# Kernel optimization log

Hardware: AMD Instinct MI355X
Metric: run time of the kernel (lower is better)

The kernel has to match this reference:

```python
import jax, jax.numpy as jnp
import numpy as np

B, T, D = 2, 4096, 2048
H, DK, DV, LR = 16, 128, 128, 16
GATE_NORM = 16.0
EPS = 1e-5
SCALE = DK ** -0.5

_PROJS = [("q", D, H * DK), ("k", D, H * DK), ("v", D, H * DV), ("g", D, H * DV), ("o", H * DV, D), ("gk0", D, LR), ("gk1", LR, H * DK)]


def setup_inputs() -> dict:
    key = jax.random.key(0)
    inp = {}
    k0, key = jax.random.split(key)
    inp["hidden_states"] = jax.random.normal(k0, (B, T, D), jnp.float32)
    for name, ind, outd in _PROJS:
        kw, ks, key = jax.random.split(key, 3)
        # int4 weights in [-8, 7], per-output-channel fp scale
        inp[name + "_w"] = jax.random.randint(kw, (outd, ind), -8, 8, dtype=jnp.int32)
        inp[name + "_wscale"] = jax.random.uniform(ks, (outd,), jnp.float32, 0.005, 0.02)
        inp[name + "_ascale"] = jnp.float32(0.05)  # per-tensor int8 activation scale
    kb, key = jax.random.split(key)
    inp["gk1_bias"] = jax.random.normal(kb, (H * DK,), jnp.float32) * 0.5
    inp["g_norm_weight"] = jnp.ones((DV,), jnp.float32)
    return inp


def _qlinear(x, w_int, wscale, ascale):
    # W4A8B16O16: symmetric per-tensor int8 activation quant (straight-through),
    # int4 weights dequantized with per-out-channel scale, fp accumulate/output.
    xq = jnp.clip(jnp.round(x / ascale), -128, 127) * ascale
    x_ste = x + jax.lax.stop_gradient(xq - x)
    w = w_int.astype(jnp.float32) * wscale[:, None]  # [out, in]
    return x_ste @ w.T


def _gla_scan(q, k, v, gk):
    # chunk_gla semantics: S_t = diag(exp(gk_t)) S_{t-1} + k_t v_t^T; o_t = (q_t * DK^-0.5) S_t
    # q,k,gk: [B,T,H,DK]; v: [B,T,H,DV]
    tm = lambda a: jnp.swapaxes(a, 0, 1)  # time-major [T,B,H,d]

    def step(S, x):
        qt, kt, vt, gt = x
        S = jnp.exp(gt)[..., None] * S + kt[..., None] * vt[..., None, :]
        return S, jnp.einsum('bhk,bhkv->bhv', qt, S)

    S0 = jnp.zeros((B, H, DK, DV), q.dtype)
    _, o = jax.lax.scan(step, S0, (tm(q) * SCALE, tm(k), tm(v), tm(gk)))
    return jnp.swapaxes(o, 0, 1)  # [B,T,H,DV]


def reference(hidden_states, q_w, q_wscale, q_ascale, k_w, k_wscale, k_ascale, v_w, v_wscale, v_ascale, g_w, g_wscale, g_ascale, o_w, o_wscale, o_ascale, gk0_w, gk0_wscale, gk0_ascale, gk1_w, gk1_wscale, gk1_ascale, gk1_bias, g_norm_weight):
    x = hidden_states
    q = _qlinear(x, q_w, q_wscale, q_ascale)
    k = _qlinear(x, k_w, k_wscale, k_ascale)
    v = _qlinear(x, v_w, v_wscale, v_ascale)
    gk = _qlinear(_qlinear(x, gk0_w, gk0_wscale, gk0_ascale), gk1_w, gk1_wscale, gk1_ascale) + gk1_bias
    rs = lambda a, d: a.reshape(*a.shape[:-1], -1, d)  # '... (h d) -> ... h d'
    q, k, gk, v = rs(q, DK), rs(k, DK), rs(gk, DK), rs(v, DV)
    gk = jax.nn.log_sigmoid(gk) / GATE_NORM
    o = _gla_scan(q, k, v, gk)
    g = rs(_qlinear(x, g_w, g_wscale, g_ascale), DV)
    # FusedRMSNormSwishGate: per-head rmsnorm(o) * weight, gated by swish(g)
    o = o * jax.lax.rsqrt(jnp.mean(o * o, axis=-1, keepdims=True) + EPS) * g_norm_weight
    o = o * (g * jax.nn.sigmoid(g))
    o = o.reshape(B, T, H * DV)
    return _qlinear(o, o_w, o_wscale, o_ascale)
```

## Files before the change

kernel.cpp:

```cpp
#include <hip/hip_runtime.h>

typedef __attribute__((ext_vector_type(4))) float f32x4;
typedef __attribute__((ext_vector_type(8))) short short8;
typedef __attribute__((ext_vector_type(4))) short short4v;
typedef __attribute__((ext_vector_type(4))) int int4v;
typedef __attribute__((ext_vector_type(8))) char char8;
typedef __attribute__((ext_vector_type(16))) char char16;
typedef unsigned int uint32;

#define DEVFN static __device__ __forceinline__
#define MFMA16x16x32 __builtin_amdgcn_mfma_f32_16x16x32_bf16
#define MFMA_I8 __builtin_amdgcn_mfma_i32_16x16x64_i8

DEVFN short f2bf_rn(float f) {
  uint32 u = __float_as_uint(f);
  u += 0x7FFFu + ((u >> 16) & 1u);
  return (short)(u >> 16);
}
DEVFN float bf2f(short s) { return __uint_as_float(((uint32)(unsigned short)s) << 16); }
DEVFN float quant1(float v, float as) {
  return fminf(fmaxf(rintf(v / as), -128.f), 127.f);
}
DEVFN void store1(float* p, float v) { *p = v; }
DEVFN void store1(short* p, float v) { *p = f2bf_rn(v); }

DEVFN void gload_lds16(const void* g, void* l) {
  __builtin_amdgcn_global_load_lds((const __attribute__((address_space(1))) void*)g,
                                   (__attribute__((address_space(3))) void*)l, 16, 0, 0);
}

__global__ __launch_bounds__(256) void repack_w_kernel(const int* __restrict__ w,
                                                       char* __restrict__ wq, int n16) {
  int stride = gridDim.x * blockDim.x;
  for (int i = blockIdx.x * blockDim.x + threadIdx.x; i < n16; i += stride) {
    char16 o;
#pragma unroll
    for (int s = 0; s < 4; s++) {
      int4v v = ((const int4v*)w)[i * 4 + s];
#pragma unroll
      for (int j = 0; j < 4; j++) o[s * 4 + j] = (char)v[j];
    }
    ((char16*)wq)[i] = o;
  }
}

__global__ __launch_bounds__(256) void quant5_kernel(
    const float* __restrict__ x, char* __restrict__ o_q, char* __restrict__ o_k,
    char* __restrict__ o_v, char* __restrict__ o_g, char* __restrict__ o_gk,
    const float* __restrict__ as_q, const float* __restrict__ as_k,
    const float* __restrict__ as_v, const float* __restrict__ as_g,
    const float* __restrict__ as_gk, int n8) {
  float aq = as_q[0], ak = as_k[0], av = as_v[0], ag = as_g[0], agk = as_gk[0];
  int stride = gridDim.x * blockDim.x;
  for (int i = blockIdx.x * blockDim.x + threadIdx.x; i < n8; i += stride) {
    f32x4 a = ((const f32x4*)x)[i * 2];
    f32x4 b = ((const f32x4*)x)[i * 2 + 1];
    float v[8] = {a.x, a.y, a.z, a.w, b.x, b.y, b.z, b.w};
    char8 q8, k8, v8, g8, gk8;
#pragma unroll
    for (int j = 0; j < 8; j++) {
      q8[j] = (char)(int)quant1(v[j], aq);
      k8[j] = (char)(int)quant1(v[j], ak);
      v8[j] = (char)(int)quant1(v[j], av);
      g8[j] = (char)(int)quant1(v[j], ag);
      gk8[j] = (char)(int)quant1(v[j], agk);
    }
    ((char8*)o_q)[i] = q8;
    ((char8*)o_k)[i] = k8;
    ((char8*)o_v)[i] = v8;
    ((char8*)o_g)[i] = g8;
    ((char8*)o_gk)[i] = gk8;
  }
}

template <typename OutT>
__global__ __launch_bounds__(512, 2) void gemm_i8(const char* __restrict__ A,
                                                  const char* __restrict__ W,
                                                  OutT* __restrict__ C,
                                                  const float* __restrict__ wscale,
                                                  const float* __restrict__ ascale_p) {
  const int K = 2048, N = 2048, NT = 32;
  int wg = blockIdx.x;
  int swz = (wg & 7) * 32 + (wg >> 3);
  int bm = swz >> 3, bn = swz & 7;

  __shared__ char As[2][256 * 64] __attribute__((aligned(16)));
  __shared__ char Bs[2][256 * 64] __attribute__((aligned(16)));

  int tid = threadIdx.x, lane = tid & 63, wid = tid >> 6;
  int wr = wid >> 2, wc = wid & 3;
  int ll = lane & 15, lh = lane >> 4;

  int4v acc[8][4];
#pragma unroll
  for (int m = 0; m < 8; m++)
#pragma unroll
    for (int n = 0; n < 4; n++) acc[m][n] = (int4v){0, 0, 0, 0};

  const char* Abase = A + (size_t)(bm * 256) * K;
  const char* Wbase = W + (size_t)(bn * 256) * K;

#define STAGE(buf, kt)                                                                   \
  {                                                                                      \
    _Pragma("unroll") for (int i = 0; i < 2; i++) {                                      \
      int rr = i * 128 + (tid >> 2);                                                     \
      int scc = (tid & 3) ^ ((rr >> 1) & 3);                                             \
      int ub = (i * 512 + wid * 64) * 16;                                                \
      gload_lds16(Abase + (size_t)rr * K + (kt) * 64 + scc * 16, (char*)As[buf] + ub);   \
      gload_lds16(Wbase + (size_t)rr * K + (kt) * 64 + scc * 16, (char*)Bs[buf] + ub);   \
    }                                                                                    \
  }

  STAGE(0, 0);
  STAGE(1, 1);
  int cur = 0;
  for (int kt = 0; kt < NT; kt++) {
    if (kt < NT - 1)
      asm volatile("s_waitcnt vmcnt(4)" ::: "memory");
    else
      asm volatile("s_waitcnt vmcnt(0)" ::: "memory");
    __builtin_amdgcn_s_barrier();
    asm volatile("" ::: "memory");
    int4v af[8], bfv[4];
#pragma unroll
    for (int m = 0; m < 8; m++) {
      int row = wr * 128 + m * 16 + ll;
      af[m] = *(const int4v*)(As[cur] + row * 64 + ((lh ^ ((row >> 1) & 3)) * 16));
    }
#pragma unroll
    for (int n = 0; n < 4; n++) {
      int row = wc * 64 + n * 16 + ll;
      bfv[n] = *(const int4v*)(Bs[cur] + row * 64 + ((lh ^ ((row >> 1) & 3)) * 16));
    }
    __builtin_amdgcn_s_setprio(1);
#pragma unroll
    for (int m = 0; m < 8; m++)
#pragma unroll
      for (int n = 0; n < 4; n++) acc[m][n] = MFMA_I8(af[m], bfv[n], acc[m][n], 0, 0, 0);
    __builtin_amdgcn_s_setprio(0);
    asm volatile("" ::: "memory");
    __builtin_amdgcn_s_barrier();
    if (kt + 2 < NT) STAGE(cur, kt + 2);
    cur ^= 1;
  }
  float as = ascale_p[0];
#pragma unroll
  for (int n = 0; n < 4; n++) {
    int col = bn * 256 + wc * 64 + n * 16 + ll;
    float sc = as * wscale[col];
#pragma unroll
    for (int m = 0; m < 8; m++) {
      int r0 = bm * 256 + wr * 128 + m * 16 + lh * 4;
#pragma unroll
      for (int j = 0; j < 4; j++) store1(C + (size_t)(r0 + j) * N + col, (float)acc[m][n][j] * sc);
    }
  }
#undef STAGE
}

__global__ __launch_bounds__(256) void gk0_kernel(const char* __restrict__ xq,
                                                  const int* __restrict__ w0,
                                                  const float* __restrict__ w0s,
                                                  const float* __restrict__ as_p,
                                                  float* __restrict__ inner) {
  const int K = 2048;
  __shared__ char W8[16 * 2064] __attribute__((aligned(16)));
  __shared__ char As[2][64 * 64] __attribute__((aligned(16)));

  int tid = threadIdx.x, lane = tid & 63, wid = tid >> 6;
  int ll = lane & 15, lh = lane >> 4;
  int bm = blockIdx.x;

#pragma unroll
  for (int i = 0; i < 32; i++) {
    int idx = i * 256 + tid;
    int4v v = ((const int4v*)w0)[idx];
    int e = idx * 4;
    char* p = W8 + (e >> 11) * 2064 + (e & 2047);
    p[0] = (char)v.x;
    p[1] = (char)v.y;
    p[2] = (char)v.z;
    p[3] = (char)v.w;
  }

  const char* Abase = xq + (size_t)(bm * 64) * K;
#define STAGEA(buf, kt)                                                              \
  {                                                                                  \
    int rr = tid >> 2, cc = tid & 3;                                                 \
    int ub = wid * 64 * 16;                                                          \
    gload_lds16(Abase + (size_t)rr * K + (kt) * 64 + cc * 16, (char*)As[buf] + ub);  \
  }

  int4v acc = (int4v){0, 0, 0, 0};
  STAGEA(0, 0);
  __syncthreads();
  int cur = 0;
  for (int kt = 0; kt < 32; kt++) {
    if (kt + 1 < 32) STAGEA(cur ^ 1, kt + 1);
    int4v bfv = *(const int4v*)(W8 + ll * 2064 + kt * 64 + lh * 16);
    int4v af = *(const int4v*)(As[cur] + (wid * 16 + ll) * 64 + lh * 16);
    acc = MFMA_I8(af, bfv, acc, 0, 0, 0);
    __syncthreads();
    cur ^= 1;
  }
  float sc = as_p[0] * w0s[ll];
  int r0 = bm * 64 + wid * 16 + lh * 4;
#pragma unroll
  for (int j = 0; j < 4; j++) inner[(size_t)(r0 + j) * 16 + ll] = (float)acc[j] * sc;
#undef STAGEA
}

__global__ __launch_bounds__(256) void gk1_kernel(const float* __restrict__ inner,
                                                  const int* __restrict__ w1,
                                                  const float* __restrict__ w1s,
                                                  const float* __restrict__ as_p,
                                                  const float* __restrict__ bias,
                                                  float* __restrict__ glog) {
  __shared__ float xq1[8][16] __attribute__((aligned(16)));
  float as = as_p[0];
  int tid = threadIdx.x;
  int m0 = blockIdx.x * 8;
  if (tid < 128) {
    int t = tid >> 4, n = tid & 15;
    xq1[t][n] = quant1(inner[(size_t)(m0 + t) * 16 + n], as);
  }
  __syncthreads();
#pragma unroll
  for (int i = 0; i < 8; i++) {
    int j = tid + i * 256;
    const int* wr = w1 + (size_t)j * 16;
    f32x4 wv[4];
#pragma unroll
    for (int n4 = 0; n4 < 4; n4++) {
      int4v wi = *(const int4v*)(wr + n4 * 4);
      wv[n4] = (f32x4){(float)wi.x, (float)wi.y, (float)wi.z, (float)wi.w};
    }
    float sc = as * w1s[j];
    float bj = bias[j];
#pragma unroll
    for (int t = 0; t < 8; t++) {
      f32x4 a4 = {0.f, 0.f, 0.f, 0.f};
#pragma unroll
      for (int n4 = 0; n4 < 4; n4++) a4 += *(const f32x4*)&xq1[t][n4 * 4] * wv[n4];
      float raw = (a4.x + a4.y + a4.z + a4.w) * sc + bj;
      float y = __expf(-fabsf(raw));
      float ls = fminf(raw, 0.f) - __logf(1.f + y);
      glog[(size_t)(m0 + t) * 2048 + j] = ls * 0.0625f;
    }
  }
}

__global__ __launch_bounds__(256) void phaseA_kernel(const float* __restrict__ Abuf,
                                                     const short* __restrict__ Kb,
                                                     const short* __restrict__ Vb,
                                                     short* __restrict__ U,
                                                     float* __restrict__ CT) {
  __shared__ short k2[16 * 128] __attribute__((aligned(16)));
  __shared__ short v2[16 * 128] __attribute__((aligned(16)));
  __shared__ short kt2[128 * 24] __attribute__((aligned(16)));
  __shared__ short vt2[128 * 24] __attribute__((aligned(16)));
  __shared__ float a_lds[16 * 136] __attribute__((aligned(16)));
  __shared__ float etot[128];

  int cid = blockIdx.x;
  int bb = cid >> 9, h = (cid >> 5) & 15, c = cid & 31;
  size_t rowbase = ((size_t)bb * 4096 + (size_t)c * 128) * 2048 + h * 128;
  int tid = threadIdx.x, lane = tid & 63, wid = tid >> 6;
  int lh = lane >> 4, ll = lane & 15;
  int r = tid >> 4, d0 = (tid & 15) * 8;

  f32x4 acc[8][2];
#pragma unroll
  for (int tm = 0; tm < 8; tm++) {
    acc[tm][0] = (f32x4){0.f, 0.f, 0.f, 0.f};
    acc[tm][1] = (f32x4){0.f, 0.f, 0.f, 0.f};
  }
  float ct[8] = {0.f, 0.f, 0.f, 0.f, 0.f, 0.f, 0.f, 0.f};

  for (int sb = 0; sb < 8; sb++) {
    __syncthreads();
    size_t ridx = rowbase + (size_t)(sb * 16 + r) * 2048 + d0;
    short8 k8 = *(const short8*)(Kb + ridx);
    short8 v8 = *(const short8*)(Vb + ridx);
    {
      f32x4 a0 = *(const f32x4*)(Abuf + ridx);
      f32x4 a1 = *(const f32x4*)(Abuf + ridx + 4);
      *(f32x4*)(a_lds + r * 136 + d0) = a0;
      *(f32x4*)(a_lds + r * 136 + d0 + 4) = a1;
    }
    __syncthreads();
    if (tid < 128) {
      int d = tid;
      float s = 0.f;
#pragma unroll
      for (int rr = 0; rr < 16; rr++) {
        s += a_lds[rr * 136 + d];
        a_lds[rr * 136 + d] = s;
      }
    }
    __syncthreads();
    {
      short8 ko;
#pragma unroll
      for (int j = 0; j < 8; j++) {
        float arel = a_lds[r * 136 + d0 + j];
        ko[j] = f2bf_rn(bf2f(k8[j]) * __expf(-arel));
        if (r == 15) {
          etot[d0 + j] = __expf(arel);
          ct[j] += arel;
        }
      }
      int byt = (r * 256 + d0 * 2) ^ ((r & 7) << 4);
      *(short8*)((char*)k2 + byt) = ko;
      *(short8*)((char*)v2 + byt) = v8;
    }
    __syncthreads();
    {
      int trow = tid >> 1, sh = (tid & 1) * 8;
      short8 tk, tv;
#pragma unroll
      for (int ss = 0; ss < 8; ss++) {
        int s = sh + ss;
        int eidx = ((s * 256 + trow * 2) ^ ((s & 7) << 4)) >> 1;
        tk[ss] = k2[eidx];
        tv[ss] = v2[eidx];
      }
      *(short8*)(kt2 + trow * 24 + sh) = tk;
      *(short8*)(vt2 + trow * 24 + sh) = tv;
    }
    __syncthreads();
    {
      int dv0 = (2 * wid) * 16 + ll, dv1 = (2 * wid + 1) * 16 + ll;
      short8 bv0 = (short8){0, 0, 0, 0, 0, 0, 0, 0}, bv1 = bv0;
      if (lh < 2) {
        bv0 = *(const short8*)(vt2 + dv0 * 24 + lh * 8);
        bv1 = *(const short8*)(vt2 + dv1 * 24 + lh * 8);
      }
#pragma unroll
      for (int tm = 0; tm < 8; tm++) {
        short8 ak = (short8){0, 0, 0, 0, 0, 0, 0, 0};
        if (lh < 2) ak = *(const short8*)(kt2 + (tm * 16 + ll) * 24 + lh * 8);
        acc[tm][0] = MFMA16x16x32(ak, bv0, acc[tm][0], 0, 0, 0);
        acc[tm][1] = MFMA16x16x32(ak, bv1, acc[tm][1], 0, 0, 0);
      }
#pragma unroll
      for (int tm = 0; tm < 8; tm++)
#pragma unroll
        for (int j = 0; j < 4; j++) {
          float e = etot[tm * 16 + lh * 4 + j];
          acc[tm][0][j] *= e;
          acc[tm][1][j] *= e;
        }
    }
  }
  size_t ub = (size_t)cid * 16384;
#pragma unroll
  for (int tm = 0; tm < 8; tm++)
#pragma unroll
    for (int tn = 0; tn < 2; tn++) {
      int dv = (2 * wid + tn) * 16 + ll;
      short4v o;
#pragma unroll
      for (int j = 0; j < 4; j++) o[j] = f2bf_rn(acc[tm][tn][j]);
      *(short4v*)(U + ub + (size_t)dv * 128 + tm * 16 + lh * 4) = o;
    }
  if (r == 15) {
#pragma unroll
    for (int j = 0; j < 8; j++) CT[(size_t)cid * 128 + d0 + j] = ct[j];
  }
}

__global__ __launch_bounds__(256) void phaseB_kernel(const float* __restrict__ CT,
                                                     short* __restrict__ US) {
  int bid = blockIdx.x;
  int bb = bid >> 7, h = (bid >> 3) & 15, dvb = bid & 7;
  int tid = threadIdx.x;
  int dv = dvb * 16 + (tid >> 4);
  int dk0 = (tid & 15) * 8;
  f32x4 s0 = {0.f, 0.f, 0.f, 0.f}, s1 = {0.f, 0.f, 0.f, 0.f};
  size_t tb = (size_t)((bb * 16 + h) * 32) * 16384 + (size_t)dv * 128 + dk0;
  size_t ctb = (size_t)((bb * 16 + h) * 32) * 128 + dk0;
  for (int c = 0; c < 32; c++) {
    size_t off = tb + (size_t)c * 16384;
    short8 u8 = *(const short8*)(US + off);
    f32x4 ea = *(const f32x4*)(CT + ctb + (size_t)c * 128);
    f32x4 eb = *(const f32x4*)(CT + ctb + (size_t)c * 128 + 4);
    short8 st;
    st[0] = f2bf_rn(s0.x); st[1] = f2bf_rn(s0.y); st[2] = f2bf_rn(s0.z); st[3] = f2bf_rn(s0.w);
    st[4] = f2bf_rn(s1.x); st[5] = f2bf_rn(s1.y); st[6] = f2bf_rn(s1.z); st[7] = f2bf_rn(s1.w);
    *(short8*)(US + off) = st;
#pragma unroll
    for (int j = 0; j < 4; j++) {
      s0[j] = __expf(ea[j]) * s0[j] + bf2f(u8[j]);
      s1[j] = __expf(eb[j]) * s1[j] + bf2f(u8[4 + j]);
    }
  }
}

__global__ __launch_bounds__(256) void phaseC_kernel(
    const float* __restrict__ Abuf, const float* __restrict__ Qb, const short* __restrict__ Kb,
    const short* __restrict__ Vb, const short* __restrict__ Gb, const short* __restrict__ S,
    const float* __restrict__ gnw, const float* __restrict__ oas_p, char* __restrict__ Oq) {
  __shared__ short st_lds[128 * 128] __attribute__((aligned(16)));
  __shared__ short q2[16 * 128] __attribute__((aligned(16)));
  __shared__ short k2[16 * 128] __attribute__((aligned(16)));
  __shared__ short v2[16 * 128] __attribute__((aligned(16)));
  __shared__ short kt2[128 * 24] __attribute__((aligned(16)));
  __shared__ short vt2[128 * 24] __attribute__((aligned(16)));
  __shared__ short p2[16 * 24] __attribute__((aligned(16)));
  __shared__ float etot[128];
  __shared__ float o_lds[16 * 136] __attribute__((aligned(16)));
  __shared__ float red[16][17];

  int cid = blockIdx.x;
  int bb = cid >> 9, h = (cid >> 5) & 15, c = cid & 31;
  size_t rowbase = ((size_t)bb * 4096 + (size_t)c * 128) * 2048 + h * 128;
  int tid = threadIdx.x, lane = tid & 63, wid = tid >> 6;
  int lh = lane >> 4, ll = lane & 15;
  float oas = oas_p[0];

  f32x4 acc[8][2];
  {
    size_t sb0 = (size_t)cid * 16384;
#pragma unroll
    for (int tm = 0; tm < 8; tm++)
#pragma unroll
      for (int tn = 0; tn < 2; tn++) {
        int dv = (2 * wid + tn) * 16 + ll;
        short4v s4 = *(const short4v*)(S + sb0 + (size_t)dv * 128 + tm * 16 + lh * 4);
        f32x4 a;
#pragma unroll
        for (int j = 0; j < 4; j++) a[j] = bf2f(s4[j]);
        acc[tm][tn] = a;
      }
  }

  int r = tid >> 4, d0 = (tid & 15) * 8;
  int t_c = tid & 15, dvb = tid >> 4;

  for (int sb = 0; sb < 8; sb++) {
    __syncthreads();
    size_t ridx = rowbase + (size_t)(sb * 16 + r) * 2048 + d0;
    f32x4 q0 = *(const f32x4*)(Qb + ridx);
    f32x4 q1 = *(const f32x4*)(Qb + ridx + 4);
    short8 k8 = *(const short8*)(Kb + ridx);
    short8 v8 = *(const short8*)(Vb + ridx);
    {
      f32x4 a0 = *(const f32x4*)(Abuf + ridx);
      f32x4 a1 = *(const f32x4*)(Abuf + ridx + 4);
      *(f32x4*)(o_lds + r * 136 + d0) = a0;
      *(f32x4*)(o_lds + r * 136 + d0 + 4) = a1;
    }
    __syncthreads();
    if (tid < 128) {
      int d = tid;
      float s = 0.f;
#pragma unroll
      for (int rr = 0; rr < 16; rr++) {
        s += o_lds[rr * 136 + d];
        o_lds[rr * 136 + d] = s;
      }
    }
    __syncthreads();
    {
      float qv[8] = {q0.x, q0.y, q0.z, q0.w, q1.x, q1.y, q1.z, q1.w};
      short8 qo, ko;
#pragma unroll
      for (int j = 0; j < 8; j++) {
        float arel = o_lds[r * 136 + d0 + j];
        float ep = __expf(arel);
        qo[j] = f2bf_rn(qv[j] * 0.08838834764831843f * ep);
        ko[j] = f2bf_rn(bf2f(k8[j]) * __expf(-arel));
        if (r == 15) etot[d0 + j] = ep;
      }
      int byt = (r * 256 + d0 * 2) ^ ((r & 7) << 4);
      *(short8*)((char*)q2 + byt) = qo;
      *(short8*)((char*)k2 + byt) = ko;
      *(short8*)((char*)v2 + byt) = v8;
    }
    __syncthreads();
    {
      int trow = tid >> 1, sh = (tid & 1) * 8;
      short8 tk, tv;
#pragma unroll
      for (int ss = 0; ss < 8; ss++) {
        int s = sh + ss;
        int eidx = ((s * 256 + trow * 2) ^ ((s & 7) << 4)) >> 1;
        tk[ss] = k2[eidx];
        tv[ss] = v2[eidx];
      }
      *(short8*)(kt2 + trow * 24 + sh) = tk;
      *(short8*)(vt2 + trow * 24 + sh) = tv;
    }
    short8 aq[4];
#pragma unroll
    for (int kk = 0; kk < 4; kk++) {
      int byt = (ll * 256 + (kk * 32 + lh * 8) * 2) ^ ((ll & 7) << 4);
      aq[kk] = *(const short8*)((char*)q2 + byt);
    }
    if (wid == 0) {
      f32x4 sc = {0.f, 0.f, 0.f, 0.f};
#pragma unroll
      for (int kk = 0; kk < 4; kk++) {
        int byt = (ll * 256 + (kk * 32 + lh * 8) * 2) ^ ((ll & 7) << 4);
        short8 bk = *(const short8*)((char*)k2 + byt);
        sc = MFMA16x16x32(aq[kk], bk, sc, 0, 0, 0);
      }
#pragma unroll
      for (int j = 0; j < 4; j++) {
        int t = lh * 4 + j;
        p2[t * 24 + ll] = f2bf_rn((ll <= t) ? sc[j] : 0.f);
      }
    }
#pragma unroll
    for (int tm = 0; tm < 8; tm++)
#pragma unroll
      for (int tn = 0; tn < 2; tn++) {
        int dv = (2 * wid + tn) * 16 + ll;
        int dkb = tm * 16 + lh * 4;
        short4v pk;
#pragma unroll
        for (int j = 0; j < 4; j++) pk[j] = f2bf_rn(acc[tm][tn][j]);
        *(short4v*)((char*)st_lds + ((dv * 256 + dkb * 2) ^ ((dv & 7) << 4))) = pk;
      }
    __syncthreads();
    {
      f32x4 oa0 = {0.f, 0.f, 0.f, 0.f}, oa1 = {0.f, 0.f, 0.f, 0.f};
      int dv0 = (2 * wid) * 16 + ll, dv1 = (2 * wid + 1) * 16 + ll;
#pragma unroll
      for (int kk = 0; kk < 4; kk++) {
        int co = (kk * 32 + lh * 8) * 2;
        short8 bs0 = *(const short8*)((char*)st_lds + ((dv0 * 256 + co) ^ ((dv0 & 7) << 4)));
        short8 bs1 = *(const short8*)((char*)st_lds + ((dv1 * 256 + co) ^ ((dv1 & 7) << 4)));
        oa0 = MFMA16x16x32(aq[kk], bs0, oa0, 0, 0, 0);
        oa1 = MFMA16x16x32(aq[kk], bs1, oa1, 0, 0, 0);
      }
      short8 ap = (short8){0, 0, 0, 0, 0, 0, 0, 0};
      short8 bv0 = ap, bv1 = ap;
      if (lh < 2) {
        ap = *(const short8*)(p2 + ll * 24 + lh * 8);
        bv0 = *(const short8*)(vt2 + dv0 * 24 + lh * 8);
        bv1 = *(const short8*)(vt2 + dv1 * 24 + lh * 8);
      }
      oa0 = MFMA16x16x32(ap, bv0, oa0, 0, 0, 0);
      oa1 = MFMA16x16x32(ap, bv1, oa1, 0, 0, 0);
#pragma unroll
      for (int j = 0; j < 4; j++) {
        o_lds[(lh * 4 + j) * 136 + dv0] = oa0[j];
        o_lds[(lh * 4 + j) * 136 + dv1] = oa1[j];
      }
    }
    {
      int dv0 = (2 * wid) * 16 + ll, dv1 = (2 * wid + 1) * 16 + ll;
      short8 bv0 = (short8){0, 0, 0, 0, 0, 0, 0, 0}, bv1 = bv0;
      if (lh < 2) {
        bv0 = *(const short8*)(vt2 + dv0 * 24 + lh * 8);
        bv1 = *(const short8*)(vt2 + dv1 * 24 + lh * 8);
      }
#pragma unroll
      for (int tm = 0; tm < 8; tm++) {
        short8 ak = (short8){0, 0, 0, 0, 0, 0, 0, 0};
        if (lh < 2) ak = *(const short8*)(kt2 + (tm * 16 + ll) * 24 + lh * 8);
        acc[tm][0] = MFMA16x16x32(ak, bv0, acc[tm][0], 0, 0, 0);
        acc[tm][1] = MFMA16x16x32(ak, bv1, acc[tm][1], 0, 0, 0);
      }
#pragma unroll
      for (int tm = 0; tm < 8; tm++)
#pragma unroll
        for (int j = 0; j < 4; j++) {
          float e = etot[tm * 16 + lh * 4 + j];
          acc[tm][0][j] *= e;
          acc[tm][1][j] *= e;
        }
    }
    __syncthreads();
    {
      f32x4 o0 = *(const f32x4*)(o_lds + t_c * 136 + dvb * 8);
      f32x4 o1 = *(const f32x4*)(o_lds + t_c * 136 + dvb * 8 + 4);
      float ov[8] = {o0.x, o0.y, o0.z, o0.w, o1.x, o1.y, o1.z, o1.w};
      float ssq = 0.f;
#pragma unroll
      for (int j = 0; j < 8; j++) ssq += ov[j] * ov[j];
      red[t_c][dvb] = ssq;
      __syncthreads();
      float tot = 0.f;
#pragma unroll
      for (int i = 0; i < 16; i++) tot += red[t_c][i];
      float rms = rsqrtf(tot * (1.f / 128.f) + 1e-5f);
      size_t gidx = rowbase + (size_t)(sb * 16 + t_c) * 2048 + dvb * 8;
      short8 g8 = *(const short8*)(Gb + gidx);
      char8 outv;
#pragma unroll
      for (int j = 0; j < 8; j++) {
        float g = bf2f(g8[j]);
        float sw = g / (1.f + __expf(-g));
        float val = ov[j] * rms * gnw[dvb * 8 + j] * sw;
        outv[j] = (char)(int)quant1(val, oas);
      }
      *(char8*)(Oq + gidx) = outv;
    }
  }
}

extern "C" void kernel_launch(void* const* d_in, const int* in_sizes, int n_in,
                              void* d_out, int out_size, void* d_ws, size_t ws_size,
                              hipStream_t stream) {
  const float* x = (const float*)d_in[0];
  const int* qw = (const int*)d_in[1];
  const float* qws = (const float*)d_in[2];
  const float* qas = (const float*)d_in[3];
  const int* kw = (const int*)d_in[4];
  const float* kws = (const float*)d_in[5];
  const float* kas = (const float*)d_in[6];
  const int* vw = (const int*)d_in[7];
  const float* vws = (const float*)d_in[8];
  const float* vas = (const float*)d_in[9];
  const int* gw = (const int*)d_in[10];
  const float* gws = (const float*)d_in[11];
  const float* gas = (const float*)d_in[12];
  const int* ow = (const int*)d_in[13];
  const float* ows = (const float*)d_in[14];
  const float* oas = (const float*)d_in[15];
  const int* gk0w = (const int*)d_in[16];
  const float* gk0ws = (const float*)d_in[17];
  const float* gk0as = (const float*)d_in[18];
  const int* gk1w = (const int*)d_in[19];
  const float* gk1ws = (const float*)d_in[20];
  const float* gk1as = (const float*)d_in[21];
  const float* gk1b = (const float*)d_in[22];
  const float* gnw = (const float*)d_in[23];

  const size_t NEEDED = 234881024ull;
  if (ws_size < NEEDED) return;

  char* ws = (char*)d_ws;
  char* WB = ws;
  char* XQq = ws + 16777216ull;
  short* KB = (short*)(ws + 33554432ull);
  short* VB = (short*)(ws + 67108864ull);
  short* GB = (short*)(ws + 100663296ull);
  char* XQk = ws + 134217728ull;
  char* XQv = ws + 150994944ull;
  char* XQg = ws + 167772160ull;
  char* XQgk = ws + 184549376ull;
  float* AB = (float*)(ws + 134217728ull);
  short* US = (short*)(ws + 201326592ull);
  float* INNER = (float*)(ws + 201326592ull);
  char* OW = ws + 201326592ull;
  float* CT = (float*)ws;
  float* QB = (float*)d_out;
  char* OQ = XQq;

  const int* wsrc[4] = {qw, kw, vw, gw};
  for (int i = 0; i < 4; i++)
    repack_w_kernel<<<1024, 256, 0, stream>>>(wsrc[i], WB + (size_t)i * 4194304, 262144);

  quant5_kernel<<<2048, 256, 0, stream>>>(x, XQq, XQk, XQv, XQg, XQgk, qas, kas, vas, gas,
                                          gk0as, 2097152);

  gemm_i8<float><<<256, 512, 0, stream>>>(XQq, WB + 0ull * 4194304, QB, qws, qas);
  gemm_i8<short><<<256, 512, 0, stream>>>(XQk, WB + 1ull * 4194304, KB, kws, kas);
  gemm_i8<short><<<256, 512, 0, stream>>>(XQv, WB + 2ull * 4194304, VB, vws, vas);
  gemm_i8<short><<<256, 512, 0, stream>>>(XQg, WB + 3ull * 4194304, GB, gws, gas);

  gk0_kernel<<<128, 256, 0, stream>>>(XQgk, gk0w, gk0ws, gk0as, INNER);
  gk1_kernel<<<1024, 256, 0, stream>>>(INNER, gk1w, gk1ws, gk1as, gk1b, AB);

  phaseA_kernel<<<1024, 256, 0, stream>>>(AB, KB, VB, US, CT);
  phaseB_kernel<<<256, 256, 0, stream>>>(CT, US);
  phaseC_kernel<<<1024, 256, 0, stream>>>(AB, QB, KB, VB, GB, US, gnw, oas, OQ);

  repack_w_kernel<<<1024, 256, 0, stream>>>(ow, OW, 262144);
  gemm_i8<float><<<256, 512, 0, stream>>>(OQ, OW, (float*)d_out, ows, oas);
}
```

Before: 560.2 us.

## Fuse per-subchunk gate cumsum into gk1 kernel, drop LDS scans in phases A/C

gk1 now processes 16 rows per block and writes a running prefix sum of the log-sigmoid gates within each 16-row subblock, instead of raw per-row gates. phaseA and phaseC then read the cumulative gate directly from global memory, which removes their shared-memory scan buffer, the serial 16-step scan, and two barriers per subblock. The cost moves into gk1, which accumulates serially across rows, and phase A's ct accumulation now relies on the last row holding the subblock total.

New measurement: 598.0 us. 6.8% more time.

```diff
diff --git a/kernel.cpp b/kernel.cpp
--- a/kernel.cpp
+++ b/kernel.cpp
@@ -216,36 +216,36 @@
                                                   const float* __restrict__ as_p,
                                                   const float* __restrict__ bias,
                                                   float* __restrict__ glog) {
-  __shared__ float xq1[8][16] __attribute__((aligned(16)));
+  __shared__ float xq1[16][16] __attribute__((aligned(16)));
   float as = as_p[0];
   int tid = threadIdx.x;
-  int m0 = blockIdx.x * 8;
-  if (tid < 128) {
+  int m0 = blockIdx.x * 16;
+  {
     int t = tid >> 4, n = tid & 15;
     xq1[t][n] = quant1(inner[(size_t)(m0 + t) * 16 + n], as);
   }
   __syncthreads();
-#pragma unroll
-  for (int i = 0; i < 8; i++) {
-    int j = tid + i * 256;
-    const int* wr = w1 + (size_t)j * 16;
+  for (int c = 0; c < 8; c++) {
+    int j = tid + c * 256;
     f32x4 wv[4];
 #pragma unroll
     for (int n4 = 0; n4 < 4; n4++) {
-      int4v wi = *(const int4v*)(wr + n4 * 4);
+      int4v wi = *(const int4v*)(w1 + (size_t)j * 16 + n4 * 4);
       wv[n4] = (f32x4){(float)wi.x, (float)wi.y, (float)wi.z, (float)wi.w};
     }
     float sc = as * w1s[j];
     float bj = bias[j];
-#pragma unroll
-    for (int t = 0; t < 8; t++) {
+    float s = 0.f;
+#pragma unroll
+    for (int r = 0; r < 16; r++) {
       f32x4 a4 = {0.f, 0.f, 0.f, 0.f};
 #pragma unroll
-      for (int n4 = 0; n4 < 4; n4++) a4 += *(const f32x4*)&xq1[t][n4 * 4] * wv[n4];
+      for (int n4 = 0; n4 < 4; n4++) a4 += *(const f32x4*)&xq1[r][n4 * 4] * wv[n4];
       float raw = (a4.x + a4.y + a4.z + a4.w) * sc + bj;
       float y = __expf(-fabsf(raw));
       float ls = fminf(raw, 0.f) - __logf(1.f + y);
-      glog[(size_t)(m0 + t) * 2048 + j] = ls * 0.0625f;
+      s += ls * 0.0625f;
+      glog[(size_t)(m0 + r) * 2048 + j] = s;
     }
   }
 }
@@ -259,7 +259,6 @@
   __shared__ short v2[16 * 128] __attribute__((aligned(16)));
   __shared__ short kt2[128 * 24] __attribute__((aligned(16)));
   __shared__ short vt2[128 * 24] __attribute__((aligned(16)));
-  __shared__ float a_lds[16 * 136] __attribute__((aligned(16)));
   __shared__ float etot[128];
 
   int cid = blockIdx.x;
@@ -279,31 +278,17 @@
 
   for (int sb = 0; sb < 8; sb++) {
     __syncthreads();
-    size_t ridx = rowbase + (size_t)(sb * 16 + r) * 2048 + d0;
-    short8 k8 = *(const short8*)(Kb + ridx);
-    short8 v8 = *(const short8*)(Vb + ridx);
-    {
+    {
+      size_t ridx = rowbase + (size_t)(sb * 16 + r) * 2048 + d0;
+      short8 k8 = *(const short8*)(Kb + ridx);
+      short8 v8 = *(const short8*)(Vb + ridx);
       f32x4 a0 = *(const f32x4*)(Abuf + ridx);
       f32x4 a1 = *(const f32x4*)(Abuf + ridx + 4);
-      *(f32x4*)(a_lds + r * 136 + d0) = a0;
-      *(f32x4*)(a_lds + r * 136 + d0 + 4) = a1;
-    }
-    __syncthreads();
-    if (tid < 128) {
-      int d = tid;
-      float s = 0.f;
-#pragma unroll
-      for (int rr = 0; rr < 16; rr++) {
-        s += a_lds[rr * 136 + d];
-        a_lds[rr * 136 + d] = s;
-      }
-    }
-    __syncthreads();
-    {
+      float av[8] = {a0.x, a0.y, a0.z, a0.w, a1.x, a1.y, a1.z, a1.w};
       short8 ko;
 #pragma unroll
       for (int j = 0; j < 8; j++) {
-        float arel = a_lds[r * 136 + d0 + j];
+        float arel = av[j];
         ko[j] = f2bf_rn(bf2f(k8[j]) * __expf(-arel));
         if (r == 15) {
           etot[d0 + j] = __expf(arel);
@@ -440,34 +425,20 @@
 
   for (int sb = 0; sb < 8; sb++) {
     __syncthreads();
-    size_t ridx = rowbase + (size_t)(sb * 16 + r) * 2048 + d0;
-    f32x4 q0 = *(const f32x4*)(Qb + ridx);
-    f32x4 q1 = *(const f32x4*)(Qb + ridx + 4);
-    short8 k8 = *(const short8*)(Kb + ridx);
-    short8 v8 = *(const short8*)(Vb + ridx);
-    {
+    {
+      size_t ridx = rowbase + (size_t)(sb * 16 + r) * 2048 + d0;
+      f32x4 q0 = *(const f32x4*)(Qb + ridx);
+      f32x4 q1 = *(const f32x4*)(Qb + ridx + 4);
+      short8 k8 = *(const short8*)(Kb + ridx);
+      short8 v8 = *(const short8*)(Vb + ridx);
       f32x4 a0 = *(const f32x4*)(Abuf + ridx);
       f32x4 a1 = *(const f32x4*)(Abuf + ridx + 4);
-      *(f32x4*)(o_lds + r * 136 + d0) = a0;
-      *(f32x4*)(o_lds + r * 136 + d0 + 4) = a1;
-    }
-    __syncthreads();
-    if (tid < 128) {
-      int d = tid;
-      float s = 0.f;
-#pragma unroll
-      for (int rr = 0; rr < 16; rr++) {
-        s += o_lds[rr * 136 + d];
-        o_lds[rr * 136 + d] = s;
-      }
-    }
-    __syncthreads();
-    {
+      float av[8] = {a0.x, a0.y, a0.z, a0.w, a1.x, a1.y, a1.z, a1.w};
       float qv[8] = {q0.x, q0.y, q0.z, q0.w, q1.x, q1.y, q1.z, q1.w};
       short8 qo, ko;
 #pragma unroll
       for (int j = 0; j < 8; j++) {
-        float arel = o_lds[r * 136 + d0 + j];
+        float arel = av[j];
         float ep = __expf(arel);
         qo[j] = f2bf_rn(qv[j] * 0.08838834764831843f * ep);
         ko[j] = f2bf_rn(bf2f(k8[j]) * __expf(-arel));
@@ -664,7 +635,7 @@
   gemm_i8<short><<<256, 512, 0, stream>>>(XQg, WB + 3ull * 4194304, GB, gws, gas);
 
   gk0_kernel<<<128, 256, 0, stream>>>(XQgk, gk0w, gk0ws, gk0as, INNER);
-  gk1_kernel<<<1024, 256, 0, stream>>>(INNER, gk1w, gk1ws, gk1as, gk1b, AB);
+  gk1_kernel<<<512, 256, 0, stream>>>(INNER, gk1w, gk1ws, gk1as, gk1b, AB);
 
   phaseA_kernel<<<1024, 256, 0, stream>>>(AB, KB, VB, US, CT);
   phaseB_kernel<<<256, 256, 0, stream>>>(CT, US);
```
